# Optimization experiments

Measured on AMD Instinct MI355X. Metric: run time of the kernel, lower is better.

Reference implementation:

```python
import jax, jax.numpy as jnp
import numpy as np

B = 32       # batch
IN_N = 32    # input capsules
IN_D = 16    # input capsule dim (== out_d)
H = 14       # input spatial
OUT_N = 32   # output capsules
OUT_D = 16
HO = 7       # parent grid h_out = w_out
HID = 64     # Linformer projection dim
EPS = 1e-5


def _gconv(x, w, groups):
    # x: [b, C, H, W], w: [C_out, C_in/groups, kh, kw]; stride 1, pad 1
    return jax.lax.conv_general_dilated(
        x, w, window_strides=(1, 1), padding=((1, 1), (1, 1)),
        dimension_numbers=("NCHW", "OIHW", "NCHW"), feature_group_count=groups)


def setup_inputs() -> dict:
    key = jax.random.key(0)
    ks = jax.random.split(key, 7)
    current_pose = jax.random.normal(ks[0], (B, IN_N, H, H, IN_D), dtype=jnp.float32)
    next_pose = jax.random.normal(ks[1], (B, OUT_N, HO, HO, OUT_D), dtype=jnp.float32)
    # grouped conv weights (torch layout OIHW, groups = IN_N)
    current_w = 0.05 * jax.random.normal(ks[2], (IN_N * IN_D, IN_D, 3, 3), dtype=jnp.float32)
    next_w = 0.05 * jax.random.normal(ks[3], (OUT_N * OUT_D, OUT_N * OUT_D // IN_N, 3, 3), dtype=jnp.float32)
    E_proj = 0.02 * jax.random.normal(ks[4], (IN_N, H * H, HID), dtype=jnp.float32)
    rel_embedd = jax.random.normal(ks[5], (IN_D, HO * HO), dtype=jnp.float32)
    ln_gamma = jnp.ones((OUT_D,), dtype=jnp.float32)
    ln_beta = jnp.zeros((OUT_D,), dtype=jnp.float32)
    return {
        "current_pose": current_pose, "next_pose": next_pose,
        "current_w": current_w, "next_w": next_w,
        "E_proj": E_proj, "rel_embedd": rel_embedd,
        "ln_gamma": ln_gamma, "ln_beta": ln_beta,
        "num_iter": 1,
    }


def reference(current_pose, next_pose, current_w, next_w, E_proj, rel_embedd,
              ln_gamma, ln_beta, num_iter):
    b = current_pose.shape[0]
    # 5D -> [b, n*d, H, W]
    cp = current_pose.transpose(0, 2, 3, 1, 4).reshape(b, H, H, IN_N * IN_D)
    cp = cp.transpose(0, 3, 1, 2)
    cp = _gconv(cp, current_w, IN_N)                       # [b, n*d, H, H]
    # headwise Linformer key projection
    cp = cp.reshape(b, IN_D, IN_N, 1, H * H)
    k = jnp.matmul(cp, E_proj)                             # [b, d, n, 1, HID]
    k = k.reshape(b, IN_D, IN_N * HID).transpose(0, 2, 1)  # [b, n*HID, d]
    rel = jnp.broadcast_to(rel_embedd.T[None], (b, HO * HO, IN_D))
    k = jnp.concatenate([k, rel], axis=1)                  # [b, N, d]

    # parent pose -> queries
    q = next_pose.transpose(0, 2, 3, 1, 4).reshape(b, HO, HO, OUT_N * OUT_D)
    q = q.transpose(0, 3, 1, 2)
    q = _gconv(q, next_w, IN_N)                            # [b, out_n*out_d, HO, HO]
    q = q.reshape(b, OUT_N * HO * HO, OUT_D)               # [b, J, d]

    dots = jnp.einsum("bje,bie->bji", q, k) * (IN_D ** -0.5)  # [b, J, N]
    dots = jax.nn.softmax(dots, axis=-2)                   # softmax over queries j
    out = jnp.einsum("bji,bie->bje", dots, k)              # [b, J, d]

    out = out.reshape(b, OUT_N * IN_D, HO, HO)
    out = _gconv(out, next_w, IN_N)
    out = out.reshape(b, OUT_N, HO, HO, IN_D)

    # LayerNorm over last dim (dropout rate = 0)
    mu = out.mean(-1, keepdims=True)
    var = ((out - mu) ** 2).mean(-1, keepdims=True)
    out = (out - mu) / jnp.sqrt(var + EPS) * ln_gamma + ln_beta
    return out
```

## Files before the change

### kernel.cpp

```cpp
#include <hip/hip_runtime.h>

typedef unsigned short u16;
typedef __attribute__((ext_vector_type(8))) short short8;
typedef __attribute__((ext_vector_type(4))) float floatx4;

#define MFMA16(a, b, c) __builtin_amdgcn_mfma_f32_16x16x32_bf16(a, b, c, 0, 0, 0)

__device__ inline u16 bf16rn(float x) {
    unsigned u = __float_as_uint(x);
    u += 0x7fffu + ((u >> 16) & 1u);
    return (u16)(u >> 16);
}
__device__ inline float bf16tof(u16 h) { return __uint_as_float(((unsigned)h) << 16); }
__device__ inline short8 ld8(const u16* p) { return *(const short8*)p; }

__global__ __launch_bounds__(256) void k_ecvt2(const float* __restrict__ E,
                                               const float* __restrict__ rel,
                                               const float* __restrict__ w,
                                               u16* __restrict__ EhT,
                                               u16* __restrict__ ElT,
                                               u16* __restrict__ Kh,
                                               u16* __restrict__ Kl,
                                               u16* __restrict__ KhT,
                                               u16* __restrict__ KlT,
                                               float* __restrict__ w2) {
    int blk = blockIdx.x, tid = threadIdx.x;
    if (blk < 32) {
        __shared__ float ep[196 * 65];
        int m = blk;
        const float* eb = E + (size_t)m * 12544;
        for (int t = tid; t < 12544; t += 256) {
            int p = t >> 6, h = t & 63;
            ep[p * 65 + h] = eb[t];
        }
        __syncthreads();
        for (int t = tid; t < 64 * 224; t += 256) {
            int h = t / 224, p = t % 224;
            float v = (p < 196) ? ep[p * 65 + h] : 0.f;
            u16 hi = bf16rn(v);
            u16 lo = bf16rn(v - bf16tof(hi));
            EhT[(size_t)m * 14336 + t] = hi;
            ElT[(size_t)m * 14336 + t] = lo;
        }
    } else if (blk < 64) {
        int b = blk - 32;
        size_t bK = (size_t)b * 2112;
        size_t bT = (size_t)b * 33792;
#pragma unroll
        for (int k = 0; k < 4; ++k) {
            int idx = tid + k * 256;
            int row = idx >> 4, e = idx & 15;
            int i = 2048 + row;
            float v = (row < 49) ? rel[e * 49 + row] : 0.f;
            u16 h = bf16rn(v);
            u16 l = bf16rn(v - bf16tof(h));
            Kh[(bK + i) * 16 + e] = h;
            Kl[(bK + i) * 16 + e] = l;
            KhT[bT + (size_t)e * 2112 + i] = h;
            KlT[bT + (size_t)e * 2112 + i] = l;
        }
    } else {
        int g0 = (blk - 64) * 4;
        for (int t = tid; t < 4 * 2304; t += 256) {
            int g = g0 + t / 2304, r = t % 2304;
            int oc = r / 144, rr = r % 144;
            w2[(size_t)g * 2304 + (rr / 9) * 144 + oc * 9 + (rr % 9)] =
                w[(size_t)g * 2304 + r];
        }
    }
}

__global__ __launch_bounds__(256) void k_conv14(const float* __restrict__ pose,
                                                const float* __restrict__ w2,
                                                float* __restrict__ out) {
    int blk = blockIdx.x;
    int oh = blk & 1, bg = blk >> 1;
    int tid = threadIdx.x;
    __shared__ float patch[16 * 256];
#pragma unroll
    for (int k = 0; k < 16; ++k) patch[k * 256 + tid] = 0.f;
    __syncthreads();
    const float* pin = pose + (size_t)bg * 3136;
    for (int t = tid; t < 3136; t += 256) {
        int p = t >> 4, ic = t & 15;
        int y = p / 14, x = p % 14;
        patch[ic * 256 + (y + 1) * 16 + (x + 1)] = pin[t];
    }
    __syncthreads();
    int g = bg & 31;
    const float* wg = w2 + (size_t)g * 2304 + oh * 72;
    float* po = out + (size_t)bg * 3136 + oh * 8 * 196;
    if (tid < 196) {
        int y = tid / 14, x = tid % 14;
        int base = (y + 1) * 16 + (x + 1);
        float acc[8];
#pragma unroll
        for (int oc = 0; oc < 8; ++oc) acc[oc] = 0.f;
        for (int ic = 0; ic < 16; ++ic) {
            const float* pr = patch + ic * 256 + base;
            float win[9];
#pragma unroll
            for (int ky = 0; ky < 3; ++ky)
#pragma unroll
                for (int kx = 0; kx < 3; ++kx)
                    win[ky * 3 + kx] = pr[(ky - 1) * 16 + (kx - 1)];
            const float* wi = wg + ic * 144;
#pragma unroll
            for (int oc = 0; oc < 8; ++oc)
#pragma unroll
                for (int kk = 0; kk < 9; ++kk)
                    acc[oc] += win[kk] * wi[oc * 9 + kk];
        }
#pragma unroll
        for (int oc = 0; oc < 8; ++oc) po[oc * 196 + tid] = acc[oc];
    }
}

__global__ __launch_bounds__(128) void k_conv7q(const float* __restrict__ pose,
                                                const float* __restrict__ w,
                                                u16* __restrict__ Qp) {
    int bg = blockIdx.x;
    int tid = threadIdx.x;
    __shared__ float patch[16 * 144];
    __shared__ float cvout[784];
    for (int t = tid; t < 16 * 144; t += 128) patch[t] = 0.f;
    __syncthreads();
    const float* pin = pose + (size_t)bg * 784;
    for (int t = tid; t < 784; t += 128) {
        int p = t >> 4, ic = t & 15;
        int y = p / 7, x = p % 7;
        patch[ic * 144 + (y + 1) * 16 + (x + 1)] = pin[t];
    }
    __syncthreads();
    int g = bg & 31;
    int oh = tid >> 6, lt = tid & 63;
    const float* wg = w + (size_t)g * 2304 + (size_t)oh * 8 * 144;
    if (lt < 49) {
        int y = lt / 7, x = lt % 7;
        int base = (y + 1) * 16 + (x + 1);
        float acc[8];
#pragma unroll
        for (int oc = 0; oc < 8; ++oc) acc[oc] = 0.f;
        for (int ic = 0; ic < 16; ++ic) {
            const float* pr = patch + ic * 144 + base;
            float win[9];
#pragma unroll
            for (int ky = 0; ky < 3; ++ky)
#pragma unroll
                for (int kx = 0; kx < 3; ++kx)
                    win[ky * 3 + kx] = pr[(ky - 1) * 16 + (kx - 1)];
            const float* wi = wg + ic * 9;
#pragma unroll
            for (int oc = 0; oc < 8; ++oc)
#pragma unroll
                for (int kk = 0; kk < 9; ++kk)
                    acc[oc] += win[kk] * wi[oc * 144 + kk];
        }
#pragma unroll
        for (int oc = 0; oc < 8; ++oc) cvout[(oh * 8 + oc) * 49 + lt] = acc[oc];
    }
    __syncthreads();
    if (tid < 49) {
        float v[16];
#pragma unroll
        for (int k = 0; k < 16; ++k) v[k] = cvout[tid * 16 + k];
        unsigned hw[8], lw[8];
#pragma unroll
        for (int t = 0; t < 8; ++t) {
            float x0 = v[2*t] * 0.25f, x1 = v[2*t+1] * 0.25f;
            u16 h0 = bf16rn(x0), h1 = bf16rn(x1);
            u16 l0 = bf16rn(x0 - bf16tof(h0)), l1 = bf16rn(x1 - bf16tof(h1));
            hw[t] = (unsigned)h0 | ((unsigned)h1 << 16);
            lw[t] = (unsigned)l0 | ((unsigned)l1 << 16);
        }
        size_t j = (size_t)bg * 49 + tid;
        uint4* r4 = (uint4*)(Qp + j * 32);
        r4[0] = make_uint4(hw[0], hw[1], hw[2], hw[3]);
        r4[1] = make_uint4(hw[4], hw[5], hw[6], hw[7]);
        r4[2] = make_uint4(lw[0], lw[1], lw[2], lw[3]);
        r4[3] = make_uint4(lw[4], lw[5], lw[6], lw[7]);
    }
}

__global__ __launch_bounds__(256) void k_kproj2(const float* __restrict__ cpconv,
                                                const u16* __restrict__ EhT,
                                                const u16* __restrict__ ElT,
                                                u16* __restrict__ Kh,
                                                u16* __restrict__ Kl,
                                                u16* __restrict__ KhT,
                                                u16* __restrict__ KlT) {
    int blk = blockIdx.x;
    int b = blk >> 5, m = blk & 31;
    int wave = threadIdx.x >> 6, lane = threadIdx.x & 63;
    int ht = wave;
    int n = lane & 15, quad = lane >> 4;

    const float* arow = cpconv + ((size_t)b * 512 + (size_t)n * 32 + m) * 196;
    const u16* bhrow = EhT + ((size_t)m * 64 + ht * 16 + n) * 224;
    const u16* blrow = ElT + ((size_t)m * 64 + ht * 16 + n) * 224;

    floatx4 c = {0.f, 0.f, 0.f, 0.f};
#pragma unroll
    for (int pc = 0; pc < 7; ++pc) {
        int p0 = pc * 32 + quad * 8;
        float av[8];
        if (p0 <= 188) {
            float4 x = *(const float4*)(arow + p0);
            float4 y = *(const float4*)(arow + p0 + 4);
            av[0]=x.x; av[1]=x.y; av[2]=x.z; av[3]=x.w;
            av[4]=y.x; av[5]=y.y; av[6]=y.z; av[7]=y.w;
        } else {
#pragma unroll
            for (int k2 = 0; k2 < 8; ++k2) av[k2] = (p0 + k2 < 196) ? arow[p0 + k2] : 0.f;
        }
        short8 ah, al;
#pragma unroll
        for (int k2 = 0; k2 < 8; ++k2) {
            u16 h = bf16rn(av[k2]);
            ah[k2] = (short)h;
            al[k2] = (short)bf16rn(av[k2] - bf16tof(h));
        }
        short8 bh = ld8(bhrow + pc * 32 + quad * 8);
        short8 bl = ld8(blrow + pc * 32 + quad * 8);
        c = MFMA16(ah, bh, c);
        c = MFMA16(ah, bl, c);
        c = MFMA16(al, bh, c);
    }
    int i = m * 64 + ht * 16 + n;
    size_t bK = (size_t)b * 2112;
    size_t bT = (size_t)b * 33792;
    u16 h[4], l[4];
#pragma unroll
    for (int r = 0; r < 4; ++r) {
        h[r] = bf16rn(c[r]);
        l[r] = bf16rn(c[r] - bf16tof(h[r]));
    }
    *(uint2*)(Kh + (bK + i) * 16 + quad * 4) =
        make_uint2((unsigned)h[0] | ((unsigned)h[1] << 16), (unsigned)h[2] | ((unsigned)h[3] << 16));
    *(uint2*)(Kl + (bK + i) * 16 + quad * 4) =
        make_uint2((unsigned)l[0] | ((unsigned)l[1] << 16), (unsigned)l[2] | ((unsigned)l[3] << 16));
#pragma unroll
    for (int r = 0; r < 4; ++r) {
        KhT[bT + (size_t)(quad * 4 + r) * 2112 + i] = h[r];
        KlT[bT + (size_t)(quad * 4 + r) * 2112 + i] = l[r];
    }
}

__global__ __launch_bounds__(256) void k_stats4(const u16* __restrict__ Qp,
                                                const u16* __restrict__ Kh,
                                                const u16* __restrict__ Kl,
                                                float* __restrict__ dpart) {
    int blk = blockIdx.x;
    int b = blk / 34; int rem = blk % 34; int jh = rem / 17; int tb = rem % 17;
    int wave = threadIdx.x >> 6, lane = threadIdx.x & 63;
    int it2 = tb * 4 + wave;
    if (it2 >= 66) return;
    int ibase = it2 * 32;
    int n = lane & 15, quad = lane >> 4;
    size_t bK = (size_t)b * 2112;
    const u16* kb = Kh + (bK + ibase + n) * 16 + (quad & 1) * 8;
    const u16* lb = Kl + (bK + ibase + n) * 16 + (quad & 1) * 8;
    short8 bh0 = ld8(kb), bh1 = ld8(kb + 256);
    short8 bl0 = ld8(lb), bl1 = ld8(lb + 256);
    const u16* qb = Qp + (size_t)b * 50176 + (size_t)jh * 49 * 512 + n * 32 + quad * 8;
    floatx4 d0 = {0.f,0.f,0.f,0.f}, d1 = {0.f,0.f,0.f,0.f};
    short8 a0 = ld8(qb), a1 = ld8(qb + 512);
    for (int c = 0; c < 49; ++c) {
        short8 a2 = (c + 2 < 49) ? ld8(qb + (size_t)(c + 2) * 512) : a0;
        floatx4 s0 = {0.f,0.f,0.f,0.f}, s1 = {0.f,0.f,0.f,0.f};
        s0 = MFMA16(a0, bh0, s0);
        s0 = MFMA16(a0, bl0, s0);
        s1 = MFMA16(a0, bh1, s1);
        s1 = MFMA16(a0, bl1, s1);
        d0.x += __expf(s0.x); d0.y += __expf(s0.y);
        d0.z += __expf(s0.z); d0.w += __expf(s0.w);
        d1.x += __expf(s1.x); d1.y += __expf(s1.y);
        d1.z += __expf(s1.z); d1.w += __expf(s1.w);
        a0 = a1; a1 = a2;
    }
    float t0 = d0.x + d0.y + d0.z + d0.w;
    float t1 = d1.x + d1.y + d1.z + d1.w;
    t0 += __shfl_xor(t0, 16); t0 += __shfl_xor(t0, 32);
    t1 += __shfl_xor(t1, 16); t1 += __shfl_xor(t1, 32);
    if (quad == 0) {
        dpart[(size_t)jh * 67584 + bK + ibase + n]      = t0;
        dpart[(size_t)jh * 67584 + bK + ibase + 16 + n] = t1;
    }
}

__global__ __launch_bounds__(256) void k_kscale(const float* __restrict__ dpart,
                                                u16* __restrict__ KhT,
                                                u16* __restrict__ KlT) {
    int blk = blockIdx.x;
    int b = blk >> 2, q = blk & 3;
    int tid = threadIdx.x;
    size_t bT = (size_t)b * 33792;
    const float* d0 = dpart + (size_t)b * 2112;
    const float* d1 = dpart + 67584 + (size_t)b * 2112;
    for (int t = tid; t < 1056; t += 256) {
        int v = q * 1056 + t;
        int e = v / 264, i8 = (v % 264) * 8;
        size_t off = bT + (size_t)e * 2112 + i8;
        uint4 hv = *(uint4*)(KhT + off);
        uint4 lv = *(uint4*)(KlT + off);
        float4 da = *(const float4*)(d0 + i8), db = *(const float4*)(d0 + i8 + 4);
        float4 ea = *(const float4*)(d1 + i8), eb = *(const float4*)(d1 + i8 + 4);
        float rl[8] = {1.f/(da.x+ea.x), 1.f/(da.y+ea.y), 1.f/(da.z+ea.z), 1.f/(da.w+ea.w),
                       1.f/(db.x+eb.x), 1.f/(db.y+eb.y), 1.f/(db.z+eb.z), 1.f/(db.w+eb.w)};
        unsigned hu[4] = {hv.x, hv.y, hv.z, hv.w};
        unsigned lu[4] = {lv.x, lv.y, lv.z, lv.w};
        unsigned ho[4], lo4[4];
#pragma unroll
        for (int k = 0; k < 4; ++k) {
            u16 h0 = (u16)hu[k], h1 = (u16)(hu[k] >> 16);
            u16 l0 = (u16)lu[k], l1 = (u16)(lu[k] >> 16);
            float v0 = (bf16tof(h0) + bf16tof(l0)) * rl[2*k];
            float v1 = (bf16tof(h1) + bf16tof(l1)) * rl[2*k+1];
            u16 nh0 = bf16rn(v0), nh1 = bf16rn(v1);
            u16 nl0 = bf16rn(v0 - bf16tof(nh0)), nl1 = bf16rn(v1 - bf16tof(nh1));
            ho[k]  = (unsigned)nh0 | ((unsigned)nh1 << 16);
            lo4[k] = (unsigned)nl0 | ((unsigned)nl1 << 16);
        }
        *(uint4*)(KhT + off) = make_uint4(ho[0], ho[1], ho[2], ho[3]);
        *(uint4*)(KlT + off) = make_uint4(lo4[0], lo4[1], lo4[2], lo4[3]);
    }
}

__global__ __launch_bounds__(256) void k_pv6(const u16* __restrict__ Qp,
                                             const u16* __restrict__ Kh,
                                             const u16* __restrict__ Kl,
                                             const u16* __restrict__ KhT,
                                             const u16* __restrict__ KlT,
                                             float* __restrict__ opart) {
    __shared__ __align__(16) u16 sH[2][32][16];
    __shared__ __align__(16) u16 sL[2][32][16];
    __shared__ __align__(16) u16 tH[2][16][32];
    __shared__ __align__(16) u16 tL[2][16][32];
    __shared__ __align__(16) u16 w16[4][2][16][40];

    int blk = blockIdx.x;
    int b = blk / 75; int rem = blk % 75; int jtb = rem / 3; int ih = rem % 3;
    int tid = threadIdx.x, wave = tid >> 6, lane = tid & 63;
    int n = lane & 15, quad = lane >> 4, qh = quad & 1;
    int jt = jtb * 4 + wave;
    int jtc = jt < 98 ? jt : 97;
    int i0 = ih * 704;
    size_t bK = (size_t)b * 2112;
    size_t bT = (size_t)b * 33792;

    short8 aq = ld8(Qp + ((size_t)b * 1568 + (size_t)jtc * 16 + n) * 32 + quad * 8);

    int role = wave, L = lane;
    uint4 sreg;
    auto ldchunk = [&](int c) {
        int i0c = i0 + c * 32;
        if (role == 0)      sreg = *(const uint4*)(Kh  + (bK + i0c + (L >> 1)) * 16 + (L & 1) * 8);
        else if (role == 1) sreg = *(const uint4*)(Kl  + (bK + i0c + (L >> 1)) * 16 + (L & 1) * 8);
        else if (role == 2) sreg = *(const uint4*)(KhT + bT + (size_t)(L >> 2) * 2112 + i0c + (L & 3) * 8);
        else                sreg = *(const uint4*)(KlT + bT + (size_t)(L >> 2) * 2112 + i0c + (L & 3) * 8);
    };
    auto stchunk = [&](int bf) {
        if (role == 0)      *(uint4*)(&sH[bf][L >> 1][(L & 1) * 8]) = sreg;
        else if (role == 1) *(uint4*)(&sL[bf][L >> 1][(L & 1) * 8]) = sreg;
        else if (role == 2) *(uint4*)(&tH[bf][L >> 2][(L & 3) * 8]) = sreg;
        else                *(uint4*)(&tL[bf][L >> 2][(L & 3) * 8]) = sreg;
    };

    floatx4 o = {0.f, 0.f, 0.f, 0.f};
    short8 thp = {}, tlp = {};

    ldchunk(0); stchunk(0); ldchunk(1);
    __syncthreads();
    for (int c = 0; c < 22; ++c) {
        int cb = c & 1;
        short8 th  = ld8(&tH[cb][n][quad * 8]);
        short8 tl  = ld8(&tL[cb][n][quad * 8]);
        short8 sh0 = ld8(&sH[cb][n][qh * 8]);
        short8 sh1 = ld8(&sH[cb][16 + n][qh * 8]);
        short8 sl0 = ld8(&sL[cb][n][qh * 8]);
        short8 sl1 = ld8(&sL[cb][16 + n][qh * 8]);
        short8 aw = {};
        if (c > 0) aw = ld8(&w16[wave][1 - cb][n][quad * 8]);
        floatx4 s0 = {0.f,0.f,0.f,0.f};
        s0 = MFMA16(aq, sh0, s0);
        s0 = MFMA16(aq, sl0, s0);
        floatx4 s1 = {0.f,0.f,0.f,0.f};
        s1 = MFMA16(aq, sh1, s1);
        s1 = MFMA16(aq, sl1, s1);
        if (c > 0) {
            o = MFMA16(aw, thp, o);
            o = MFMA16(aw, tlp, o);
        }
#pragma unroll
        for (int r = 0; r < 4; ++r) {
            float w0 = __expf(s0[r]);
            float w1 = __expf(s1[r]);
            w16[wave][cb][quad * 4 + r][n]      = (u16)(__float_as_uint(w0) >> 16);
            w16[wave][cb][quad * 4 + r][16 + n] = (u16)(__float_as_uint(w1) >> 16);
        }
        thp = th; tlp = tl;
        if (c + 1 < 22) stchunk((c + 1) & 1);
        if (c + 2 < 22) ldchunk(c + 2);
        __syncthreads();
    }
    {
        short8 aw = ld8(&w16[wave][1][n][quad * 8]);
        o = MFMA16(aw, thp, o);
        o = MFMA16(aw, tlp, o);
    }
    if (jt < 98) {
        float* ob = opart + (size_t)ih * 802816 + ((size_t)b * 1568 + (size_t)jt * 16) * 16;
#pragma unroll
        for (int r = 0; r < 4; ++r) ob[(quad * 4 + r) * 16 + n] = o[r];
    }
}

__global__ __launch_bounds__(128) void k_conv7ln(const float* __restrict__ op0,
                                                 const float* __restrict__ op1,
                                                 const float* __restrict__ op2,
                                                 const float* __restrict__ w,
                                                 const float* __restrict__ gamma,
                                                 const float* __restrict__ beta,
                                                 float* __restrict__ out) {
    int bg = blockIdx.x;
    int tid = threadIdx.x;
    __shared__ float patch[16 * 144];
    __shared__ float cvout[784];
    for (int t = tid; t < 16 * 144; t += 128) patch[t] = 0.f;
    __syncthreads();
    const float* p0 = op0 + (size_t)bg * 784;
    const float* p1 = op1 + (size_t)bg * 784;
    const float* p2 = op2 + (size_t)bg * 784;
    for (int t = tid; t < 784; t += 128) {
        int ic = t / 49, p = t % 49;
        int y = p / 7, x = p % 7;
        patch[ic * 144 + (y + 1) * 16 + (x + 1)] = p0[t] + p1[t] + p2[t];
    }
    __syncthreads();
    int g = bg & 31;
    int oh = tid >> 6, lt = tid & 63;
    const float* wg = w + (size_t)g * 2304 + (size_t)oh * 8 * 144;
    if (lt < 49) {
        int y = lt / 7, x = lt % 7;
        int base = (y + 1) * 16 + (x + 1);
        float acc[8];
#pragma unroll
        for (int oc = 0; oc < 8; ++oc) acc[oc] = 0.f;
        for (int ic = 0; ic < 16; ++ic) {
            const float* pr = patch + ic * 144 + base;
            float win[9];
#pragma unroll
            for (int ky = 0; ky < 3; ++ky)
#pragma unroll
                for (int kx = 0; kx < 3; ++kx)
                    win[ky * 3 + kx] = pr[(ky - 1) * 16 + (kx - 1)];
            const float* wi = wg + ic * 9;
#pragma unroll
            for (int oc = 0; oc < 8; ++oc)
#pragma unroll
                for (int kk = 0; kk < 9; ++kk)
                    acc[oc] += win[kk] * wi[oc * 144 + kk];
        }
#pragma unroll
        for (int oc = 0; oc < 8; ++oc) cvout[(oh * 8 + oc) * 49 + lt] = acc[oc];
    }
    __syncthreads();
    if (tid < 49) {
        float v[16];
        float sum = 0.f;
#pragma unroll
        for (int k = 0; k < 16; ++k) { v[k] = cvout[tid * 16 + k]; sum += v[k]; }
        float mu = sum * 0.0625f;
        float var = 0.f;
#pragma unroll
        for (int k = 0; k < 16; ++k) { float d = v[k] - mu; var += d * d; }
        float rstd = rsqrtf(var * 0.0625f + 1e-5f);
        float4 o4[4];
#pragma unroll
        for (int k = 0; k < 16; ++k)
            ((float*)o4)[k] = (v[k] - mu) * rstd * gamma[k] + beta[k];
        float4* po = (float4*)(out + (size_t)bg * 784 + (size_t)tid * 16);
        po[0] = o4[0]; po[1] = o4[1]; po[2] = o4[2]; po[3] = o4[3];
    }
}

extern "C" void kernel_launch(void* const* d_in, const int* in_sizes, int n_in,
                              void* d_out, int out_size, void* d_ws, size_t ws_size,
                              hipStream_t stream) {
    const float* current_pose = (const float*)d_in[0];
    const float* next_pose    = (const float*)d_in[1];
    const float* current_w    = (const float*)d_in[2];
    const float* next_w       = (const float*)d_in[3];
    const float* E_proj       = (const float*)d_in[4];
    const float* rel          = (const float*)d_in[5];
    const float* ln_gamma     = (const float*)d_in[6];
    const float* ln_beta      = (const float*)d_in[7];
    float* out = (float*)d_out;
    float* ws  = (float*)d_ws;

    float* cpconv = ws;
    float* opart  = ws;
    float* dpart  = ws + 2408448;
    float* w2     = ws + 3211264;
    u16*   ub     = (u16*)(ws + 3284992);
    u16* Qp  = ub;
    u16* Kh  = ub + 1605632;
    u16* Kl  = ub + 2686976;
    u16* KhT = ub + 3768320;
    u16* KlT = ub + 4849664;
    u16* EhT = ub + 5931008;
    u16* ElT = ub + 6389760;

    k_ecvt2  <<<72,   256, 0, stream>>>(E_proj, rel, current_w, EhT, ElT,
                                        Kh, Kl, KhT, KlT, w2);
    k_conv14 <<<2048, 256, 0, stream>>>(current_pose, w2, cpconv);
    k_conv7q <<<1024, 128, 0, stream>>>(next_pose, next_w, Qp);
    k_kproj2 <<<1024, 256, 0, stream>>>(cpconv, EhT, ElT, Kh, Kl, KhT, KlT);
    k_stats4 <<<1088, 256, 0, stream>>>(Qp, Kh, Kl, dpart);
    k_kscale <<<128,  256, 0, stream>>>(dpart, KhT, KlT);
    k_pv6    <<<2400, 256, 0, stream>>>(Qp, Kh, Kl, KhT, KlT, opart);
    k_conv7ln<<<1024, 128, 0, stream>>>(opart, opart + 802816, opart + 1605632,
                                        next_w, ln_gamma, ln_beta, out);
    (void)in_sizes; (void)n_in; (void)out_size; (void)ws_size;
}
```

Measured before the change: 235.9 us.

## Fuse prep convs into one kernel, fold softmax scaling into PV, use exp2

Merges the weight/E conversion, 14x14 conv and 7x7 query conv into a single prep kernel. The 14x14 conv now writes split bf16 hi/lo directly, so the key-projection kernel skips its fp32 loads and conversion. The separate k_kscale pass is dropped: reciprocal column sums are loaded alongside K chunks and applied to the exp weights inside the PV kernel. Exponentials switch to exp2 with a log2e-folded query scale. LDS arrays are padded to reduce bank conflicts. The cost is a more heterogeneous prep kernel with larger shared memory, and extra per-chunk reciprocal work in PV.

```diff
diff --git a/kernel.cpp b/kernel.cpp
--- a/kernel.cpp
+++ b/kernel.cpp
@@ -13,176 +13,185 @@
 }
 __device__ inline float bf16tof(u16 h) { return __uint_as_float(((unsigned)h) << 16); }
 __device__ inline short8 ld8(const u16* p) { return *(const short8*)p; }
-
-__global__ __launch_bounds__(256) void k_ecvt2(const float* __restrict__ E,
-                                               const float* __restrict__ rel,
-                                               const float* __restrict__ w,
-                                               u16* __restrict__ EhT,
-                                               u16* __restrict__ ElT,
-                                               u16* __restrict__ Kh,
-                                               u16* __restrict__ Kl,
-                                               u16* __restrict__ KhT,
-                                               u16* __restrict__ KlT,
-                                               float* __restrict__ w2) {
+__device__ inline float exp2fast(float x) { return __builtin_amdgcn_exp2f(x); }
+
+#define QSC 0.36067376022224085f
+
+__global__ __launch_bounds__(256) void k_prep(const float* __restrict__ pose14,
+                                              const float* __restrict__ pose7,
+                                              const float* __restrict__ E,
+                                              const float* __restrict__ rel,
+                                              const float* __restrict__ cw,
+                                              const float* __restrict__ nw,
+                                              u16* __restrict__ cph,
+                                              u16* __restrict__ cpl,
+                                              u16* __restrict__ Qp,
+                                              u16* __restrict__ EhT,
+                                              u16* __restrict__ ElT,
+                                              u16* __restrict__ Kh,
+                                              u16* __restrict__ Kl,
+                                              u16* __restrict__ KhT,
+                                              u16* __restrict__ KlT) {
+    __shared__ __align__(16) float smem[6400];
     int blk = blockIdx.x, tid = threadIdx.x;
-    if (blk < 32) {
-        __shared__ float ep[196 * 65];
-        int m = blk;
-        const float* eb = E + (size_t)m * 12544;
-        for (int t = tid; t < 12544; t += 256) {
-            int p = t >> 6, h = t & 63;
-            ep[p * 65 + h] = eb[t];
-        }
-        __syncthreads();
-        for (int t = tid; t < 64 * 224; t += 256) {
-            int h = t / 224, p = t % 224;
-            float v = (p < 196) ? ep[p * 65 + h] : 0.f;
-            u16 hi = bf16rn(v);
-            u16 lo = bf16rn(v - bf16tof(hi));
-            EhT[(size_t)m * 14336 + t] = hi;
-            ElT[(size_t)m * 14336 + t] = lo;
-        }
-    } else if (blk < 64) {
-        int b = blk - 32;
-        size_t bK = (size_t)b * 2112;
-        size_t bT = (size_t)b * 33792;
-#pragma unroll
-        for (int k = 0; k < 4; ++k) {
-            int idx = tid + k * 256;
-            int row = idx >> 4, e = idx & 15;
-            int i = 2048 + row;
-            float v = (row < 49) ? rel[e * 49 + row] : 0.f;
-            u16 h = bf16rn(v);
-            u16 l = bf16rn(v - bf16tof(h));
-            Kh[(bK + i) * 16 + e] = h;
-            Kl[(bK + i) * 16 + e] = l;
-            KhT[bT + (size_t)e * 2112 + i] = h;
-            KlT[bT + (size_t)e * 2112 + i] = l;
+
+    if (blk < 2048) {
+        int oh = blk & 1, bg = blk >> 1;
+        float* patch = smem;
+#pragma unroll
+        for (int k = 0; k < 16; ++k) patch[k * 256 + tid] = 0.f;
+        __syncthreads();
+        const float* pin = pose14 + (size_t)bg * 3136;
+        for (int t = tid; t < 3136; t += 256) {
+            int p = t >> 4, ic = t & 15;
+            int y = p / 14, x = p % 14;
+            patch[ic * 256 + (y + 1) * 16 + (x + 1)] = pin[t];
+        }
+        __syncthreads();
+        int g = bg & 31;
+        const float* wg = cw + (size_t)g * 2304 + (size_t)oh * 8 * 144;
+        if (tid < 196) {
+            int y = tid / 14, x = tid % 14;
+            int base = (y + 1) * 16 + (x + 1);
+            float acc[8];
+#pragma unroll
+            for (int oc = 0; oc < 8; ++oc) acc[oc] = 0.f;
+            for (int ic = 0; ic < 16; ++ic) {
+                const float* pr = patch + ic * 256 + base;
+                float win[9];
+#pragma unroll
+                for (int ky = 0; ky < 3; ++ky)
+#pragma unroll
+                    for (int kx = 0; kx < 3; ++kx)
+                        win[ky * 3 + kx] = pr[(ky - 1) * 16 + (kx - 1)];
+#pragma unroll
+                for (int oc = 0; oc < 8; ++oc)
+#pragma unroll
+                    for (int kk = 0; kk < 9; ++kk)
+                        acc[oc] += win[kk] * wg[oc * 144 + ic * 9 + kk];
+            }
+#pragma unroll
+            for (int oc = 0; oc < 8; ++oc) {
+                size_t row = (size_t)bg * 16 + oh * 8 + oc;
+                u16 h = bf16rn(acc[oc]);
+                cph[row * 224 + tid] = h;
+                cpl[row * 224 + tid] = bf16rn(acc[oc] - bf16tof(h));
+            }
+        }
+    } else if (blk < 2560) {
+        int idx = blk - 2048, half = tid >> 7, t128 = tid & 127;
+        int bg = idx * 2 + half;
+        float* patch = smem + half * 2304;
+        float* cvq   = smem + 4608 + half * 832;
+        for (int t = t128; t < 2304; t += 128) patch[t] = 0.f;
+        __syncthreads();
+        const float* pin = pose7 + (size_t)bg * 784;
+        for (int t = t128; t < 784; t += 128) {
+            int p = t >> 4, ic = t & 15;
+            int y = p / 7, x = p % 7;
+            patch[ic * 144 + (y + 1) * 16 + (x + 1)] = pin[t];
+        }
+        __syncthreads();
+        int g = bg & 31;
+        int oh = t128 >> 6, lt = t128 & 63;
+        const float* wg = nw + (size_t)g * 2304 + (size_t)oh * 8 * 144;
+        if (lt < 49) {
+            int y = lt / 7, x = lt % 7;
+            int base = (y + 1) * 16 + (x + 1);
+            float acc[8];
+#pragma unroll
+            for (int oc = 0; oc < 8; ++oc) acc[oc] = 0.f;
+            for (int ic = 0; ic < 16; ++ic) {
+                const float* pr = patch + ic * 144 + base;
+                float win[9];
+#pragma unroll
+                for (int ky = 0; ky < 3; ++ky)
+#pragma unroll
+                    for (int kx = 0; kx < 3; ++kx)
+                        win[ky * 3 + kx] = pr[(ky - 1) * 16 + (kx - 1)];
+#pragma unroll
+                for (int oc = 0; oc < 8; ++oc)
+#pragma unroll
+                    for (int kk = 0; kk < 9; ++kk)
+                        acc[oc] += win[kk] * wg[oc * 144 + ic * 9 + kk];
+            }
+#pragma unroll
+            for (int oc = 0; oc < 8; ++oc) {
+                int f = (oh * 8 + oc) * 49 + lt;
+                cvq[(f & 15) * 52 + (f >> 4)] = acc[oc];
+            }
+        }
+        __syncthreads();
+        if (t128 < 49) {
+            float v[16];
+#pragma unroll
+            for (int k = 0; k < 16; ++k) v[k] = cvq[k * 52 + t128];
+            unsigned hw[8], lw[8];
+#pragma unroll
+            for (int t = 0; t < 8; ++t) {
+                float x0 = v[2*t] * QSC, x1 = v[2*t+1] * QSC;
+                u16 h0 = bf16rn(x0), h1 = bf16rn(x1);
+                u16 l0 = bf16rn(x0 - bf16tof(h0)), l1 = bf16rn(x1 - bf16tof(h1));
+                hw[t] = (unsigned)h0 | ((unsigned)h1 << 16);
+                lw[t] = (unsigned)l0 | ((unsigned)l1 << 16);
+            }
+            size_t j = (size_t)bg * 49 + t128;
+            uint4* r4 = (uint4*)(Qp + j * 32);
+            r4[0] = make_uint4(hw[0], hw[1], hw[2], hw[3]);
+            r4[1] = make_uint4(hw[4], hw[5], hw[6], hw[7]);
+            r4[2] = make_uint4(lw[0], lw[1], lw[2], lw[3]);
+            r4[3] = make_uint4(lw[4], lw[5], lw[6], lw[7]);
         }
     } else {
-        int g0 = (blk - 64) * 4;
-        for (int t = tid; t < 4 * 2304; t += 256) {
-            int g = g0 + t / 2304, r = t % 2304;
-            int oc = r / 144, rr = r % 144;
-            w2[(size_t)g * 2304 + (rr / 9) * 144 + oc * 9 + (rr % 9)] =
-                w[(size_t)g * 2304 + r];
-        }
-    }
-}
-
-__global__ __launch_bounds__(256) void k_conv14(const float* __restrict__ pose,
-                                                const float* __restrict__ w2,
-                                                float* __restrict__ out) {
-    int blk = blockIdx.x;
-    int oh = blk & 1, bg = blk >> 1;
-    int tid = threadIdx.x;
-    __shared__ float patch[16 * 256];
-#pragma unroll
-    for (int k = 0; k < 16; ++k) patch[k * 256 + tid] = 0.f;
-    __syncthreads();
-    const float* pin = pose + (size_t)bg * 3136;
-    for (int t = tid; t < 3136; t += 256) {
-        int p = t >> 4, ic = t & 15;
-        int y = p / 14, x = p % 14;
-        patch[ic * 256 + (y + 1) * 16 + (x + 1)] = pin[t];
-    }
-    __syncthreads();
-    int g = bg & 31;
-    const float* wg = w2 + (size_t)g * 2304 + oh * 72;
-    float* po = out + (size_t)bg * 3136 + oh * 8 * 196;
-    if (tid < 196) {
-        int y = tid / 14, x = tid % 14;
-        int base = (y + 1) * 16 + (x + 1);
-        float acc[8];
-#pragma unroll
-        for (int oc = 0; oc < 8; ++oc) acc[oc] = 0.f;
-        for (int ic = 0; ic < 16; ++ic) {
-            const float* pr = patch + ic * 256 + base;
-            float win[9];
-#pragma unroll
-            for (int ky = 0; ky < 3; ++ky)
-#pragma unroll
-                for (int kx = 0; kx < 3; ++kx)
-                    win[ky * 3 + kx] = pr[(ky - 1) * 16 + (kx - 1)];
-            const float* wi = wg + ic * 144;
-#pragma unroll
-            for (int oc = 0; oc < 8; ++oc)
-#pragma unroll
-                for (int kk = 0; kk < 9; ++kk)
-                    acc[oc] += win[kk] * wi[oc * 9 + kk];
-        }
-#pragma unroll
-        for (int oc = 0; oc < 8; ++oc) po[oc * 196 + tid] = acc[oc];
-    }
-}
-
-__global__ __launch_bounds__(128) void k_conv7q(const float* __restrict__ pose,
-                                                const float* __restrict__ w,
-                                                u16* __restrict__ Qp) {
-    int bg = blockIdx.x;
-    int tid = threadIdx.x;
-    __shared__ float patch[16 * 144];
-    __shared__ float cvout[784];
-    for (int t = tid; t < 16 * 144; t += 128) patch[t] = 0.f;
-    __syncthreads();
-    const float* pin = pose + (size_t)bg * 784;
-    for (int t = tid; t < 784; t += 128) {
-        int p = t >> 4, ic = t & 15;
-        int y = p / 7, x = p % 7;
-        patch[ic * 144 + (y + 1) * 16 + (x + 1)] = pin[t];
-    }
-    __syncthreads();
-    int g = bg & 31;
-    int oh = tid >> 6, lt = tid & 63;
-    const float* wg = w + (size_t)g * 2304 + (size_t)oh * 8 * 144;
-    if (lt < 49) {
-        int y = lt / 7, x = lt % 7;
-        int base = (y + 1) * 16 + (x + 1);
-        float acc[8];
-#pragma unroll
-        for (int oc = 0; oc < 8; ++oc) acc[oc] = 0.f;
-        for (int ic = 0; ic < 16; ++ic) {
-            const float* pr = patch + ic * 144 + base;
-            float win[9];
-#pragma unroll
-            for (int ky = 0; ky < 3; ++ky)
-#pragma unroll
-                for (int kx = 0; kx < 3; ++kx)
-                    win[ky * 3 + kx] = pr[(ky - 1) * 16 + (kx - 1)];
-            const float* wi = wg + ic * 9;
-#pragma unroll
-            for (int oc = 0; oc < 8; ++oc)
-#pragma unroll
-                for (int kk = 0; kk < 9; ++kk)
-                    acc[oc] += win[kk] * wi[oc * 144 + kk];
-        }
-#pragma unroll
-        for (int oc = 0; oc < 8; ++oc) cvout[(oh * 8 + oc) * 49 + lt] = acc[oc];
-    }
-    __syncthreads();
-    if (tid < 49) {
-        float v[16];
-#pragma unroll
-        for (int k = 0; k < 16; ++k) v[k] = cvout[tid * 16 + k];
-        unsigned hw[8], lw[8];
-#pragma unroll
-        for (int t = 0; t < 8; ++t) {
-            float x0 = v[2*t] * 0.25f, x1 = v[2*t+1] * 0.25f;
-            u16 h0 = bf16rn(x0), h1 = bf16rn(x1);
-            u16 l0 = bf16rn(x0 - bf16tof(h0)), l1 = bf16rn(x1 - bf16tof(h1));
-            hw[t] = (unsigned)h0 | ((unsigned)h1 << 16);
-            lw[t] = (unsigned)l0 | ((unsigned)l1 << 16);
-        }
-        size_t j = (size_t)bg * 49 + tid;
-        uint4* r4 = (uint4*)(Qp + j * 32);
-        r4[0] = make_uint4(hw[0], hw[1], hw[2], hw[3]);
-        r4[1] = make_uint4(hw[4], hw[5], hw[6], hw[7]);
-        r4[2] = make_uint4(lw[0], lw[1], lw[2], lw[3]);
-        r4[3] = make_uint4(lw[4], lw[5], lw[6], lw[7]);
-    }
-}
-
-__global__ __launch_bounds__(256) void k_kproj2(const float* __restrict__ cpconv,
+        int e = blk - 2560;
+        if (e < 32) {
+            int m = e;
+            const float* eb = E + (size_t)m * 12544;
+            u16* po = EhT + (size_t)m * 14336;
+            u16* pl = ElT + (size_t)m * 14336;
+            for (int pt = 0; pt < 4; ++pt) {
+                int pbase = pt * 49;
+                for (int t = tid; t < 3136; t += 256) {
+                    int p = t >> 6, h = t & 63;
+                    smem[p * 65 + h] = eb[(size_t)(pbase + p) * 64 + h];
+                }
+                __syncthreads();
+                for (int t = tid; t < 3136; t += 256) {
+                    int h = t / 49, p = t % 49;
+                    float v = smem[p * 65 + h];
+                    u16 hi = bf16rn(v);
+                    po[h * 224 + pbase + p] = hi;
+                    pl[h * 224 + pbase + p] = bf16rn(v - bf16tof(hi));
+                }
+                __syncthreads();
+            }
+            for (int t = tid; t < 64 * 28; t += 256) {
+                int h = t / 28, p = 196 + t % 28;
+                po[h * 224 + p] = 0; pl[h * 224 + p] = 0;
+            }
+        } else {
+            int b = e - 32;
+            size_t bK = (size_t)b * 2112;
+            size_t bT = (size_t)b * 33792;
+#pragma unroll
+            for (int k = 0; k < 4; ++k) {
+                int idx = tid + k * 256;
+                int row = idx >> 4, ee = idx & 15;
+                int i = 2048 + row;
+                float v = (row < 49) ? rel[ee * 49 + row] : 0.f;
+                u16 h = bf16rn(v);
+                u16 l = bf16rn(v - bf16tof(h));
+                Kh[(bK + i) * 16 + ee] = h;
+                Kl[(bK + i) * 16 + ee] = l;
+                KhT[bT + (size_t)ee * 2112 + i] = h;
+                KlT[bT + (size_t)ee * 2112 + i] = l;
+            }
+        }
+    }
+}
+
+__global__ __launch_bounds__(256) void k_kproj2(const u16* __restrict__ cph,
+                                                const u16* __restrict__ cpl,
                                                 const u16* __restrict__ EhT,
                                                 const u16* __restrict__ ElT,
                                                 u16* __restrict__ Kh,
@@ -195,7 +204,8 @@
     int ht = wave;
     int n = lane & 15, quad = lane >> 4;
 
-    const float* arow = cpconv + ((size_t)b * 512 + (size_t)n * 32 + m) * 196;
+    const u16* ahrow = cph + ((size_t)b * 512 + (size_t)n * 32 + m) * 224;
+    const u16* alrow = cpl + ((size_t)b * 512 + (size_t)n * 32 + m) * 224;
     const u16* bhrow = EhT + ((size_t)m * 64 + ht * 16 + n) * 224;
     const u16* blrow = ElT + ((size_t)m * 64 + ht * 16 + n) * 224;
 
@@ -203,25 +213,10 @@
 #pragma unroll
     for (int pc = 0; pc < 7; ++pc) {
         int p0 = pc * 32 + quad * 8;
-        float av[8];
-        if (p0 <= 188) {
-            float4 x = *(const float4*)(arow + p0);
-            float4 y = *(const float4*)(arow + p0 + 4);
-            av[0]=x.x; av[1]=x.y; av[2]=x.z; av[3]=x.w;
-            av[4]=y.x; av[5]=y.y; av[6]=y.z; av[7]=y.w;
-        } else {
-#pragma unroll
-            for (int k2 = 0; k2 < 8; ++k2) av[k2] = (p0 + k2 < 196) ? arow[p0 + k2] : 0.f;
-        }
-        short8 ah, al;
-#pragma unroll
-        for (int k2 = 0; k2 < 8; ++k2) {
-            u16 h = bf16rn(av[k2]);
-            ah[k2] = (short)h;
-            al[k2] = (short)bf16rn(av[k2] - bf16tof(h));
-        }
-        short8 bh = ld8(bhrow + pc * 32 + quad * 8);
-        short8 bl = ld8(blrow + pc * 32 + quad * 8);
+        short8 ah = ld8(ahrow + p0);
+        short8 al = ld8(alrow + p0);
+        short8 bh = ld8(bhrow + p0);
+        short8 bl = ld8(blrow + p0);
         c = MFMA16(ah, bh, c);
         c = MFMA16(ah, bl, c);
         c = MFMA16(al, bh, c);
@@ -246,7 +241,7 @@
     }
 }
 
-__global__ __launch_bounds__(256) void k_stats4(const u16* __restrict__ Qp,
+__global__ __launch_bounds__(256) void k_stats5(const u16* __restrict__ Qp,
                                                 const u16* __restrict__ Kh,
                                                 const u16* __restrict__ Kl,
                                                 float* __restrict__ dpart) {
@@ -272,10 +267,10 @@
         s0 = MFMA16(a0, bl0, s0);
         s1 = MFMA16(a0, bh1, s1);
         s1 = MFMA16(a0, bl1, s1);
-        d0.x += __expf(s0.x); d0.y += __expf(s0.y);
-        d0.z += __expf(s0.z); d0.w += __expf(s0.w);
-        d1.x += __expf(s1.x); d1.y += __expf(s1.y);
-        d1.z += __expf(s1.z); d1.w += __expf(s1.w);
+        d0.x += exp2fast(s0.x); d0.y += exp2fast(s0.y);
+        d0.z += exp2fast(s0.z); d0.w += exp2fast(s0.w);
+        d1.x += exp2fast(s1.x); d1.y += exp2fast(s1.y);
+        d1.z += exp2fast(s1.z); d1.w += exp2fast(s1.w);
         a0 = a1; a1 = a2;
     }
     float t0 = d0.x + d0.y + d0.z + d0.w;
@@ -288,55 +283,19 @@
     }
 }
 
-__global__ __launch_bounds__(256) void k_kscale(const float* __restrict__ dpart,
-                                                u16* __restrict__ KhT,
-                                                u16* __restrict__ KlT) {
-    int blk = blockIdx.x;
-    int b = blk >> 2, q = blk & 3;
-    int tid = threadIdx.x;
-    size_t bT = (size_t)b * 33792;
-    const float* d0 = dpart + (size_t)b * 2112;
-    const float* d1 = dpart + 67584 + (size_t)b * 2112;
-    for (int t = tid; t < 1056; t += 256) {
-        int v = q * 1056 + t;
-        int e = v / 264, i8 = (v % 264) * 8;
-        size_t off = bT + (size_t)e * 2112 + i8;
-        uint4 hv = *(uint4*)(KhT + off);
-        uint4 lv = *(uint4*)(KlT + off);
-        float4 da = *(const float4*)(d0 + i8), db = *(const float4*)(d0 + i8 + 4);
-        float4 ea = *(const float4*)(d1 + i8), eb = *(const float4*)(d1 + i8 + 4);
-        float rl[8] = {1.f/(da.x+ea.x), 1.f/(da.y+ea.y), 1.f/(da.z+ea.z), 1.f/(da.w+ea.w),
-                       1.f/(db.x+eb.x), 1.f/(db.y+eb.y), 1.f/(db.z+eb.z), 1.f/(db.w+eb.w)};
-        unsigned hu[4] = {hv.x, hv.y, hv.z, hv.w};
-        unsigned lu[4] = {lv.x, lv.y, lv.z, lv.w};
-        unsigned ho[4], lo4[4];
-#pragma unroll
-        for (int k = 0; k < 4; ++k) {
-            u16 h0 = (u16)hu[k], h1 = (u16)(hu[k] >> 16);
-            u16 l0 = (u16)lu[k], l1 = (u16)(lu[k] >> 16);
-            float v0 = (bf16tof(h0) + bf16tof(l0)) * rl[2*k];
-            float v1 = (bf16tof(h1) + bf16tof(l1)) * rl[2*k+1];
-            u16 nh0 = bf16rn(v0), nh1 = bf16rn(v1);
-            u16 nl0 = bf16rn(v0 - bf16tof(nh0)), nl1 = bf16rn(v1 - bf16tof(nh1));
-            ho[k]  = (unsigned)nh0 | ((unsigned)nh1 << 16);
-            lo4[k] = (unsigned)nl0 | ((unsigned)nl1 << 16);
-        }
-        *(uint4*)(KhT + off) = make_uint4(ho[0], ho[1], ho[2], ho[3]);
-        *(uint4*)(KlT + off) = make_uint4(lo4[0], lo4[1], lo4[2], lo4[3]);
-    }
-}
-
-__global__ __launch_bounds__(256) void k_pv6(const u16* __restrict__ Qp,
+__global__ __launch_bounds__(256) void k_pv7(const u16* __restrict__ Qp,
                                              const u16* __restrict__ Kh,
                                              const u16* __restrict__ Kl,
                                              const u16* __restrict__ KhT,
                                              const u16* __restrict__ KlT,
+                                             const float* __restrict__ dpart,
                                              float* __restrict__ opart) {
-    __shared__ __align__(16) u16 sH[2][32][16];
-    __shared__ __align__(16) u16 sL[2][32][16];
-    __shared__ __align__(16) u16 tH[2][16][32];
-    __shared__ __align__(16) u16 tL[2][16][32];
+    __shared__ __align__(16) u16 sH[2][32][24];
+    __shared__ __align__(16) u16 sL[2][32][24];
+    __shared__ __align__(16) u16 tH[2][16][40];
+    __shared__ __align__(16) u16 tL[2][16][40];
     __shared__ __align__(16) u16 w16[4][2][16][40];
+    __shared__ float rll[2][32];
 
     int blk = blockIdx.x;
     int b = blk / 75; int rem = blk % 75; int jtb = rem / 3; int ih = rem % 3;
@@ -347,23 +306,31 @@
     int i0 = ih * 704;
     size_t bK = (size_t)b * 2112;
     size_t bT = (size_t)b * 33792;
+    const float* d0p = dpart + bK;
+    const float* d1p = dpart + 67584 + bK;
 
     short8 aq = ld8(Qp + ((size_t)b * 1568 + (size_t)jtc * 16 + n) * 32 + quad * 8);
 
     int role = wave, L = lane;
-    uint4 sreg;
+    uint4 sreg; float rv = 0.f;
     auto ldchunk = [&](int c) {
         int i0c = i0 + c * 32;
         if (role == 0)      sreg = *(const uint4*)(Kh  + (bK + i0c + (L >> 1)) * 16 + (L & 1) * 8);
         else if (role == 1) sreg = *(const uint4*)(Kl  + (bK + i0c + (L >> 1)) * 16 + (L & 1) * 8);
         else if (role == 2) sreg = *(const uint4*)(KhT + bT + (size_t)(L >> 2) * 2112 + i0c + (L & 3) * 8);
-        else                sreg = *(const uint4*)(KlT + bT + (size_t)(L >> 2) * 2112 + i0c + (L & 3) * 8);
+        else {
+            sreg = *(const uint4*)(KlT + bT + (size_t)(L >> 2) * 2112 + i0c + (L & 3) * 8);
+            if (L < 32) rv = 1.0f / (d0p[i0c + L] + d1p[i0c + L]);
+        }
     };
     auto stchunk = [&](int bf) {
         if (role == 0)      *(uint4*)(&sH[bf][L >> 1][(L & 1) * 8]) = sreg;
         else if (role == 1) *(uint4*)(&sL[bf][L >> 1][(L & 1) * 8]) = sreg;
         else if (role == 2) *(uint4*)(&tH[bf][L >> 2][(L & 3) * 8]) = sreg;
-        else                *(uint4*)(&tL[bf][L >> 2][(L & 3) * 8]) = sreg;
+        else {
+            *(uint4*)(&tL[bf][L >> 2][(L & 3) * 8]) = sreg;
+            if (L < 32) rll[bf][L] = rv;
+        }
     };
 
     floatx4 o = {0.f, 0.f, 0.f, 0.f};
@@ -379,6 +346,7 @@
         short8 sh1 = ld8(&sH[cb][16 + n][qh * 8]);
         short8 sl0 = ld8(&sL[cb][n][qh * 8]);
         short8 sl1 = ld8(&sL[cb][16 + n][qh * 8]);
+        float r0 = rll[cb][n], r1 = rll[cb][16 + n];
         short8 aw = {};
         if (c > 0) aw = ld8(&w16[wave][1 - cb][n][quad * 8]);
         floatx4 s0 = {0.f,0.f,0.f,0.f};
@@ -393,13 +361,13 @@
         }
 #pragma unroll
         for (int r = 0; r < 4; ++r) {
-            float w0 = __expf(s0[r]);
-            float w1 = __expf(s1[r]);
+            float w0 = exp2fast(s0[r]) * r0;
+            float w1 = exp2fast(s1[r]) * r1;
             w16[wave][cb][quad * 4 + r][n]      = (u16)(__float_as_uint(w0) >> 16);
             w16[wave][cb][quad * 4 + r][16 + n] = (u16)(__float_as_uint(w1) >> 16);
         }
         thp = th; tlp = tl;
-        if (c + 1 < 22) stchunk((c + 1) & 1);
+        if (c + 1 < 22) stchunk(cb ^ 1);
         if (c + 2 < 22) ldchunk(c + 2);
         __syncthreads();
     }
@@ -425,7 +393,7 @@
     int bg = blockIdx.x;
     int tid = threadIdx.x;
     __shared__ float patch[16 * 144];
-    __shared__ float cvout[784];
+    __shared__ float cvout[16][52];
     for (int t = tid; t < 16 * 144; t += 128) patch[t] = 0.f;
     __syncthreads();
     const float* p0 = op0 + (size_t)bg * 784;
@@ -454,22 +422,24 @@
 #pragma unroll
                 for (int kx = 0; kx < 3; ++kx)
                     win[ky * 3 + kx] = pr[(ky - 1) * 16 + (kx - 1)];
-            const float* wi = wg + ic * 9;
 #pragma unroll
             for (int oc = 0; oc < 8; ++oc)
 #pragma unroll
                 for (int kk = 0; kk < 9; ++kk)
-                    acc[oc] += win[kk] * wi[oc * 144 + kk];
-        }
-#pragma unroll
-        for (int oc = 0; oc < 8; ++oc) cvout[(oh * 8 + oc) * 49 + lt] = acc[oc];
+                    acc[oc] += win[kk] * wg[oc * 144 + ic * 9 + kk];
+        }
+#pragma unroll
+        for (int oc = 0; oc < 8; ++oc) {
+            int f = (oh * 8 + oc) * 49 + lt;
+            cvout[f & 15][f >> 4] = acc[oc];
+        }
     }
     __syncthreads();
     if (tid < 49) {
         float v[16];
         float sum = 0.f;
 #pragma unroll
-        for (int k = 0; k < 16; ++k) { v[k] = cvout[tid * 16 + k]; sum += v[k]; }
+        for (int k = 0; k < 16; ++k) { v[k] = cvout[k][tid]; sum += v[k]; }
         float mu = sum * 0.0625f;
         float var = 0.f;
 #pragma unroll
@@ -498,11 +468,11 @@
     float* out = (float*)d_out;
     float* ws  = (float*)d_ws;
 
-    float* cpconv = ws;
-    float* opart  = ws;
-    float* dpart  = ws + 2408448;
-    float* w2     = ws + 3211264;
-    u16*   ub     = (u16*)(ws + 3284992);
+    u16*   cph   = (u16*)ws;
+    u16*   cpl   = cph + 3670016;
+    float* opart = ws;
+    float* dpart = ws + 3670016;
+    u16*   ub    = (u16*)(ws + 3805184);
     u16* Qp  = ub;
     u16* Kh  = ub + 1605632;
     u16* Kl  = ub + 2686976;
@@ -511,14 +481,12 @@
     u16* EhT = ub + 5931008;
     u16* ElT = ub + 6389760;
 
-    k_ecvt2  <<<72,   256, 0, stream>>>(E_proj, rel, current_w, EhT, ElT,
-                                        Kh, Kl, KhT, KlT, w2);
-    k_conv14 <<<2048, 256, 0, stream>>>(current_pose, w2, cpconv);
-    k_conv7q <<<1024, 128, 0, stream>>>(next_pose, next_w, Qp);
-    k_kproj2 <<<1024, 256, 0, stream>>>(cpconv, EhT, ElT, Kh, Kl, KhT, KlT);
-    k_stats4 <<<1088, 256, 0, stream>>>(Qp, Kh, Kl, dpart);
-    k_kscale <<<128,  256, 0, stream>>>(dpart, KhT, KlT);
-    k_pv6    <<<2400, 256, 0, stream>>>(Qp, Kh, Kl, KhT, KlT, opart);
+    k_prep   <<<2624, 256, 0, stream>>>(current_pose, next_pose, E_proj, rel,
+                                        current_w, next_w, cph, cpl, Qp,
+                                        EhT, ElT, Kh, Kl, KhT, KlT);
+    k_kproj2 <<<1024, 256, 0, stream>>>(cph, cpl, EhT, ElT, Kh, Kl, KhT, KlT);
+    k_stats5 <<<1088, 256, 0, stream>>>(Qp, Kh, Kl, dpart);
+    k_pv7    <<<2400, 256, 0, stream>>>(Qp, Kh, Kl, KhT, KlT, dpart, opart);
     k_conv7ln<<<1024, 128, 0, stream>>>(opart, opart + 802816, opart + 1605632,
                                         next_w, ln_gamma, ln_beta, out);
     (void)in_sizes; (void)n_in; (void)out_size; (void)ws_size;
```

Result: slower. 242.3 us (+2.7%).
